# Performance work log

Measured on AMD Instinct MI355X. Metric: run time of the kernel, lower is better.

## Reference

```python
import jax, jax.numpy as jnp
import numpy as np

D_MODEL = 512
N_HEADS = 8
D_K = D_MODEL // N_HEADS
B = 16
S = 1024


def setup_inputs() -> dict:
    key = jax.random.key(0)
    ks = jax.random.split(key, 9)
    xavier = (2.0 / (D_MODEL + D_MODEL)) ** 0.5  # xavier_normal std for square proj
    x = jax.random.normal(ks[0], (B, S, D_MODEL), dtype=jnp.float32)
    Wq = jax.random.normal(ks[1], (D_MODEL, D_MODEL), dtype=jnp.float32) * xavier
    Wk = jax.random.normal(ks[2], (D_MODEL, D_MODEL), dtype=jnp.float32) * xavier
    Wv = jax.random.normal(ks[3], (D_MODEL, D_MODEL), dtype=jnp.float32) * xavier
    Wo = jax.random.normal(ks[4], (D_MODEL, D_MODEL), dtype=jnp.float32) * xavier
    bq = jnp.zeros((D_MODEL,), jnp.float32)
    bk = jnp.zeros((D_MODEL,), jnp.float32)
    bv = jnp.zeros((D_MODEL,), jnp.float32)
    bo = jnp.zeros((D_MODEL,), jnp.float32)
    return {"x": x, "Wq": Wq, "bq": bq, "Wk": Wk, "bk": bk,
            "Wv": Wv, "bv": bv, "Wo": Wo, "bo": bo}


def reference(x, Wq, bq, Wk, bk, Wv, bv, Wo, bo):
    # x: (B, S, D). Projections (nn.Linear applies x @ W.T + b; here W stored as (in,out)).
    b, s, _ = x.shape
    def split_heads(t):  # (B,S,D) -> (B,H,S,dk)
        return t.reshape(b, s, N_HEADS, D_K).transpose(0, 2, 1, 3)
    Q = split_heads(x @ Wq + bq)
    K = split_heads(x @ Wk + bk)
    V = split_heads(x @ Wv + bv)
    scale = 1.0 / jnp.sqrt(jnp.asarray(D_K, x.dtype))
    scores = jnp.einsum('bhqd,bhkd->bhqk', Q, K) * scale
    attn_weights = jax.nn.softmax(scores, axis=-1)
    # dropout is identity in eval mode
    ctx = jnp.einsum('bhqk,bhkd->bhqd', attn_weights, V)
    ctx = ctx.transpose(0, 2, 1, 3).reshape(b, s, D_MODEL)
    out = ctx @ Wo + bo
    return out, attn_weights
```

## Files before the change

kernel.cpp:

```cpp
#include <hip/hip_runtime.h>
#include <stdint.h>

#define D_MODELC 512
#define N_HEADSC 8
#define DKH 64
#define BATCH 16
#define SEQ 1024
#define M_TOT (BATCH*SEQ)
#define NBH (BATCH*N_HEADSC)

typedef __attribute__((ext_vector_type(8))) short short8;
typedef __attribute__((ext_vector_type(4))) float float4v;
typedef __attribute__((ext_vector_type(4))) unsigned short ushort4v;

__device__ inline unsigned short f2bf(float f) {
    unsigned u = __float_as_uint(f);
    u += 0x7FFFu + ((u >> 16) & 1u);
    return (unsigned short)(u >> 16);
}

__device__ inline void gl2lds16(const void* g, void* l) {
    __builtin_amdgcn_global_load_lds(
        (__attribute__((address_space(1))) void*)g,
        (__attribute__((address_space(3))) void*)l, 16, 0, 0);
}

__global__ void k_cvt_x(const float* __restrict__ x, unsigned short* __restrict__ xb) {
    int i = (blockIdx.x * 256 + threadIdx.x) * 4;
    float4v v = *(const float4v*)(x + i);
    ushort4v o;
    o.x = f2bf(v.x); o.y = f2bf(v.y); o.z = f2bf(v.z); o.w = f2bf(v.w);
    *(ushort4v*)(xb + i) = o;
}

__global__ void k_wt(const float* __restrict__ Wq, const float* __restrict__ Wk,
                     const float* __restrict__ Wv, const float* __restrict__ Wo,
                     unsigned short* __restrict__ Wqkvt, unsigned short* __restrict__ Wot) {
    __shared__ float tile[32][33];
    const int blk = blockIdx.x;
    const int mat = blk >> 8;
    const int t2  = blk & 255;
    const int kt = (t2 >> 4) * 32;
    const int nt = (t2 & 15) * 32;
    const float* W = mat == 0 ? Wq : mat == 1 ? Wk : mat == 2 ? Wv : Wo;
    const int tid = threadIdx.x;
    const int cx = tid & 31, ry = tid >> 5;
#pragma unroll
    for (int p = 0; p < 4; ++p) {
        int kr = ry + p * 8;
        tile[kr][cx] = W[(size_t)(kt + kr) * 512 + nt + cx];
    }
    __syncthreads();
    unsigned short* DST = (mat < 3) ? (Wqkvt + (size_t)mat * 512 * 512) : Wot;
#pragma unroll
    for (int p = 0; p < 4; ++p) {
        int nr = ry + p * 8;
        DST[(size_t)(nt + nr) * 512 + kt + cx] = f2bf(tile[cx][nr]);
    }
}

template<int MODE>
__global__ __launch_bounds__(256, 2) void k_gemm(
    const unsigned short* __restrict__ A,
    const unsigned short* __restrict__ Bt,
    const float* __restrict__ bias0,
    const float* __restrict__ bias1,
    const float* __restrict__ bias2,
    unsigned short* __restrict__ Qb,
    unsigned short* __restrict__ Kb,
    unsigned short* __restrict__ Vtb,
    float* __restrict__ Out)
{
    __shared__ __align__(16) unsigned short As[128 * 32];
    __shared__ __align__(16) unsigned short Bs[128 * 32];
    const int m0 = blockIdx.y * 128;
    const int n0 = blockIdx.x * 128;
    const int tid = threadIdx.x;
    const int w = tid >> 6, l = tid & 63;
    const int lm = l & 15, q4 = l >> 4;
    const int wm = (w >> 1) * 64, wn = (w & 1) * 64;

    float4v acc[4][4] = {};

    for (int k0 = 0; k0 < 512; k0 += 32) {
#pragma unroll
        for (int r = 0; r < 2; ++r) {
            int e = tid * 8 + r * 2048;
            int row = e >> 5, col = e & 31;
            gl2lds16(A  + (size_t)(m0 + row) * 512 + k0 + col,
                     (char*)As + w * 1024 + r * 4096);
            gl2lds16(Bt + (size_t)(n0 + row) * 512 + k0 + col,
                     (char*)Bs + w * 1024 + r * 4096);
        }
        __syncthreads();
        short8 af[4], bfr[4];
#pragma unroll
        for (int mi = 0; mi < 4; ++mi)
            af[mi] = *(const short8*)(As + (wm + mi * 16 + lm) * 32 + q4 * 8);
#pragma unroll
        for (int ni = 0; ni < 4; ++ni)
            bfr[ni] = *(const short8*)(Bs + (wn + ni * 16 + lm) * 32 + q4 * 8);
#pragma unroll
        for (int mi = 0; mi < 4; ++mi)
#pragma unroll
            for (int ni = 0; ni < 4; ++ni)
                acc[mi][ni] = __builtin_amdgcn_mfma_f32_16x16x32_bf16(
                    af[mi], bfr[ni], acc[mi][ni], 0, 0, 0);
        __syncthreads();
    }

#pragma unroll
    for (int mi = 0; mi < 4; ++mi)
#pragma unroll
        for (int ni = 0; ni < 4; ++ni)
#pragma unroll
            for (int r = 0; r < 4; ++r) {
                int m = m0 + wm + mi * 16 + q4 * 4 + r;
                int n = n0 + wn + ni * 16 + lm;
                float v = acc[mi][ni][r];
                if (MODE == 0) {
                    int which = n >> 9;
                    int nn = n & 511;
                    int h = nn >> 6, d = nn & 63;
                    int b = m >> 10, s = m & 1023;
                    size_t qkoff = (((size_t)(b * N_HEADSC + h)) * SEQ + s) * DKH + d;
                    if (which == 0) {
                        v = (v + bias0[nn]) * 0.125f;
                        Qb[qkoff] = f2bf(v);
                    } else if (which == 1) {
                        Kb[qkoff] = f2bf(v + bias1[nn]);
                    } else {
                        Vtb[(((size_t)(b * N_HEADSC + h)) * DKH + d) * SEQ + s] =
                            f2bf(v + bias2[nn]);
                    }
                } else {
                    Out[(size_t)m * 512 + n] = v + bias0[n];
                }
            }
}

__global__ __launch_bounds__(256, 2) void k_attn(
    const unsigned short* __restrict__ Qb,
    const unsigned short* __restrict__ Kb,
    float* __restrict__ attn)
{
    __shared__ float wstat[4][32];
    const int blk = blockIdx.x;
    const int bh = blk >> 5;
    const int m0 = (blk & 31) * 32;
    const int tid = threadIdx.x;
    const int w = tid >> 6, l = tid & 63;
    const int lm = l & 15, q4 = l >> 4;
    const unsigned short* Qh = Qb + (size_t)bh * SEQ * DKH;
    const unsigned short* Kh = Kb + (size_t)bh * SEQ * DKH;
    const int nw0 = w * 256;

    short8 a[2][2];
#pragma unroll
    for (int mi = 0; mi < 2; ++mi)
#pragma unroll
        for (int ks = 0; ks < 2; ++ks)
            a[mi][ks] = *(const short8*)(Qh + (size_t)(m0 + mi * 16 + lm) * 64 + ks * 32 + q4 * 8);

    float4v acc[2][16];
#pragma unroll
    for (int cg = 0; cg < 16; ++cg) {
        const unsigned short* kp = Kh + (size_t)(nw0 + cg * 16 + lm) * 64 + q4 * 8;
        short8 b0 = *(const short8*)kp;
        short8 b1 = *(const short8*)(kp + 32);
#pragma unroll
        for (int mi = 0; mi < 2; ++mi) {
            float4v z = {0.f, 0.f, 0.f, 0.f};
            z = __builtin_amdgcn_mfma_f32_16x16x32_bf16(a[mi][0], b0, z, 0, 0, 0);
            acc[mi][cg] = __builtin_amdgcn_mfma_f32_16x16x32_bf16(a[mi][1], b1, z, 0, 0, 0);
        }
    }

    float gM[2][4];
#pragma unroll
    for (int mi = 0; mi < 2; ++mi)
#pragma unroll
        for (int r = 0; r < 4; ++r) {
            float pm = -1e30f;
#pragma unroll
            for (int cg = 0; cg < 16; ++cg) pm = fmaxf(pm, acc[mi][cg][r]);
#pragma unroll
            for (int sh = 1; sh < 16; sh <<= 1) pm = fmaxf(pm, __shfl_xor(pm, sh));
            gM[mi][r] = pm;
        }
    if (lm == 0) {
#pragma unroll
        for (int mi = 0; mi < 2; ++mi)
#pragma unroll
            for (int r = 0; r < 4; ++r)
                wstat[w][mi * 16 + q4 * 4 + r] = gM[mi][r];
    }
    __syncthreads();
#pragma unroll
    for (int mi = 0; mi < 2; ++mi)
#pragma unroll
        for (int r = 0; r < 4; ++r) {
            int row = mi * 16 + q4 * 4 + r;
            gM[mi][r] = fmaxf(fmaxf(wstat[0][row], wstat[1][row]),
                              fmaxf(wstat[2][row], wstat[3][row]));
        }
    __syncthreads();

    float gS[2][4];
#pragma unroll
    for (int mi = 0; mi < 2; ++mi)
#pragma unroll
        for (int r = 0; r < 4; ++r) {
            float ps = 0.f;
#pragma unroll
            for (int cg = 0; cg < 16; ++cg) {
                float e = __expf(acc[mi][cg][r] - gM[mi][r]);
                acc[mi][cg][r] = e;
                ps += e;
            }
#pragma unroll
            for (int sh = 1; sh < 16; sh <<= 1) ps += __shfl_xor(ps, sh);
            gS[mi][r] = ps;
        }
    if (lm == 0) {
#pragma unroll
        for (int mi = 0; mi < 2; ++mi)
#pragma unroll
            for (int r = 0; r < 4; ++r)
                wstat[w][mi * 16 + q4 * 4 + r] = gS[mi][r];
    }
    __syncthreads();
    float inv[2][4];
#pragma unroll
    for (int mi = 0; mi < 2; ++mi)
#pragma unroll
        for (int r = 0; r < 4; ++r) {
            int row = mi * 16 + q4 * 4 + r;
            inv[mi][r] = 1.f / (wstat[0][row] + wstat[1][row] + wstat[2][row] + wstat[3][row]);
        }

    const size_t base = (size_t)bh * SEQ * SEQ;
#pragma unroll
    for (int cg = 0; cg < 16; ++cg)
#pragma unroll
        for (int mi = 0; mi < 2; ++mi)
#pragma unroll
            for (int r = 0; r < 4; ++r)
                attn[base + (size_t)(m0 + mi * 16 + q4 * 4 + r) * SEQ + nw0 + cg * 16 + lm] =
                    acc[mi][cg][r] * inv[mi][r];
}

__global__ __launch_bounds__(256, 2) void k_pv(
    const float* __restrict__ attn,
    const unsigned short* __restrict__ Vtb,
    unsigned short* __restrict__ ctx)
{
    const int blk = blockIdx.x;
    const int bh = blk >> 3;
    const int m0 = (blk & 7) * 128;
    const int tid = threadIdx.x;
    const int w = tid >> 6, l = tid & 63;
    const int lm = l & 15, q4 = l >> 4;
    const float* Ph = attn + (size_t)bh * SEQ * SEQ;
    const unsigned short* Vh = Vtb + (size_t)bh * DKH * SEQ;
    const int wm = w * 32;

    float4v acc[2][4] = {};
    for (int kc = 0; kc < 1024; kc += 32) {
        short8 a[2];
#pragma unroll
        for (int mi = 0; mi < 2; ++mi) {
            const float* p = Ph + (size_t)(m0 + wm + mi * 16 + lm) * SEQ + kc + q4 * 8;
            float4v p0 = *(const float4v*)p;
            float4v p1 = *(const float4v*)(p + 4);
            short8 t;
            t[0] = (short)f2bf(p0.x); t[1] = (short)f2bf(p0.y);
            t[2] = (short)f2bf(p0.z); t[3] = (short)f2bf(p0.w);
            t[4] = (short)f2bf(p1.x); t[5] = (short)f2bf(p1.y);
            t[6] = (short)f2bf(p1.z); t[7] = (short)f2bf(p1.w);
            a[mi] = t;
        }
#pragma unroll
        for (int ni = 0; ni < 4; ++ni) {
            short8 bfr = *(const short8*)(Vh + (size_t)(ni * 16 + lm) * SEQ + kc + q4 * 8);
#pragma unroll
            for (int mi = 0; mi < 2; ++mi)
                acc[mi][ni] = __builtin_amdgcn_mfma_f32_16x16x32_bf16(a[mi], bfr, acc[mi][ni], 0, 0, 0);
        }
    }
    const int bb = bh >> 3, h = bh & 7;
#pragma unroll
    for (int mi = 0; mi < 2; ++mi)
#pragma unroll
        for (int ni = 0; ni < 4; ++ni)
#pragma unroll
            for (int r = 0; r < 4; ++r) {
                int s = m0 + wm + mi * 16 + q4 * 4 + r;
                int d = ni * 16 + lm;
                ctx[((size_t)(bb * SEQ + s)) * 512 + h * 64 + d] = f2bf(acc[mi][ni][r]);
            }
}

extern "C" void kernel_launch(void* const* d_in, const int* in_sizes, int n_in,
                              void* d_out, int out_size, void* d_ws, size_t ws_size,
                              hipStream_t stream) {
    const float* x  = (const float*)d_in[0];
    const float* Wq = (const float*)d_in[1];
    const float* bq = (const float*)d_in[2];
    const float* Wk = (const float*)d_in[3];
    const float* bk = (const float*)d_in[4];
    const float* Wv = (const float*)d_in[5];
    const float* bv = (const float*)d_in[6];
    const float* Wo = (const float*)d_in[7];
    const float* bo = (const float*)d_in[8];

    float* out  = (float*)d_out;
    float* attn = out + (size_t)M_TOT * D_MODELC;

    char* ws = (char*)d_ws;
    unsigned short* xb    = (unsigned short*)(ws);
    unsigned short* Qb    = (unsigned short*)(ws + (size_t)(16u << 20));
    unsigned short* Kb    = (unsigned short*)(ws + (size_t)(32u << 20));
    unsigned short* Vtb   = (unsigned short*)(ws + (size_t)(48u << 20));
    unsigned short* ctxb  = (unsigned short*)(ws + (size_t)(64u << 20));
    unsigned short* Wqkvt = (unsigned short*)(ws + (size_t)(80u << 20));
    unsigned short* Wot   = (unsigned short*)(ws + (size_t)(82u << 20));

    k_cvt_x<<<8192, 256, 0, stream>>>(x, xb);
    k_wt<<<1024, 256, 0, stream>>>(Wq, Wk, Wv, Wo, Wqkvt, Wot);
    k_gemm<0><<<dim3(12, 128), 256, 0, stream>>>(xb, Wqkvt, bq, bk, bv,
                                                 Qb, Kb, Vtb, nullptr);
    k_attn<<<4096, 256, 0, stream>>>(Qb, Kb, attn);
    k_pv<<<1024, 256, 0, stream>>>(attn, Vtb, ctxb);
    k_gemm<1><<<dim3(4, 128), 256, 0, stream>>>(ctxb, Wot, bo, nullptr, nullptr,
                                                nullptr, nullptr, nullptr, out);
}
```

Measured before the change: 951.8 us.

## Fuse PV matmul into attention kernel using LDS-staged bf16 probabilities

Merges the softmax/attention-weights kernel and the P·V kernel into one. Each block writes the normalized probabilities to global memory as before and also stores them as bf16 in a swizzled LDS buffer. It then computes the context for its 32 query rows directly from LDS, so the separate kernel no longer has to re-read the 512MB fp32 attention matrix. The cost is 64KB of LDS per block, which may lower occupancy below the declared two blocks per CU. V is also re-read per 32-row block instead of per 128-row block.

```diff
diff --git a/kernel.cpp b/kernel.cpp
--- a/kernel.cpp
+++ b/kernel.cpp
@@ -139,20 +139,24 @@
             }
 }
 
-__global__ __launch_bounds__(256, 2) void k_attn(
+__global__ __launch_bounds__(256, 2) void k_attn_pv(
     const unsigned short* __restrict__ Qb,
     const unsigned short* __restrict__ Kb,
-    float* __restrict__ attn)
+    const unsigned short* __restrict__ Vtb,
+    float* __restrict__ attn,
+    unsigned short* __restrict__ ctx)
 {
     __shared__ float wstat[4][32];
+    __shared__ __align__(16) unsigned short Pl[4][32 * 256];
     const int blk = blockIdx.x;
     const int bh = blk >> 5;
     const int m0 = (blk & 31) * 32;
     const int tid = threadIdx.x;
     const int w = tid >> 6, l = tid & 63;
     const int lm = l & 15, q4 = l >> 4;
-    const unsigned short* Qh = Qb + (size_t)bh * SEQ * DKH;
-    const unsigned short* Kh = Kb + (size_t)bh * SEQ * DKH;
+    const unsigned short* Qh = Qb  + (size_t)bh * SEQ * DKH;
+    const unsigned short* Kh = Kb  + (size_t)bh * SEQ * DKH;
+    const unsigned short* Vh = Vtb + (size_t)bh * DKH * SEQ;
     const int nw0 = w * 256;
 
     short8 a[2][2];
@@ -240,65 +244,49 @@
         }
 
     const size_t base = (size_t)bh * SEQ * SEQ;
-#pragma unroll
-    for (int cg = 0; cg < 16; ++cg)
-#pragma unroll
-        for (int mi = 0; mi < 2; ++mi)
-#pragma unroll
-            for (int r = 0; r < 4; ++r)
-                attn[base + (size_t)(m0 + mi * 16 + q4 * 4 + r) * SEQ + nw0 + cg * 16 + lm] =
-                    acc[mi][cg][r] * inv[mi][r];
-}
-
-__global__ __launch_bounds__(256, 2) void k_pv(
-    const float* __restrict__ attn,
-    const unsigned short* __restrict__ Vtb,
-    unsigned short* __restrict__ ctx)
-{
-    const int blk = blockIdx.x;
-    const int bh = blk >> 3;
-    const int m0 = (blk & 7) * 128;
-    const int tid = threadIdx.x;
-    const int w = tid >> 6, l = tid & 63;
-    const int lm = l & 15, q4 = l >> 4;
-    const float* Ph = attn + (size_t)bh * SEQ * SEQ;
-    const unsigned short* Vh = Vtb + (size_t)bh * DKH * SEQ;
-    const int wm = w * 32;
-
-    float4v acc[2][4] = {};
-    for (int kc = 0; kc < 1024; kc += 32) {
-        short8 a[2];
-#pragma unroll
-        for (int mi = 0; mi < 2; ++mi) {
-            const float* p = Ph + (size_t)(m0 + wm + mi * 16 + lm) * SEQ + kc + q4 * 8;
-            float4v p0 = *(const float4v*)p;
-            float4v p1 = *(const float4v*)(p + 4);
-            short8 t;
-            t[0] = (short)f2bf(p0.x); t[1] = (short)f2bf(p0.y);
-            t[2] = (short)f2bf(p0.z); t[3] = (short)f2bf(p0.w);
-            t[4] = (short)f2bf(p1.x); t[5] = (short)f2bf(p1.y);
-            t[6] = (short)f2bf(p1.z); t[7] = (short)f2bf(p1.w);
-            a[mi] = t;
-        }
-#pragma unroll
-        for (int ni = 0; ni < 4; ++ni) {
-            short8 bfr = *(const short8*)(Vh + (size_t)(ni * 16 + lm) * SEQ + kc + q4 * 8);
-#pragma unroll
-            for (int mi = 0; mi < 2; ++mi)
-                acc[mi][ni] = __builtin_amdgcn_mfma_f32_16x16x32_bf16(a[mi], bfr, acc[mi][ni], 0, 0, 0);
+    char* Pw = (char*)&Pl[w][0];
+#pragma unroll
+    for (int mi = 0; mi < 2; ++mi)
+#pragma unroll
+        for (int r = 0; r < 4; ++r) {
+            const int row = mi * 16 + q4 * 4 + r;
+            const int rx = (row & 7) << 4;
+            const float iv = inv[mi][r];
+            float* arow = attn + base + (size_t)(m0 + row) * SEQ + nw0;
+#pragma unroll
+            for (int cg = 0; cg < 16; ++cg) {
+                float p = acc[mi][cg][r] * iv;
+                arow[cg * 16 + lm] = p;
+                *(unsigned short*)(Pw + row * 512 + (((cg * 16 + lm) * 2) ^ rx)) = f2bf(p);
+            }
+        }
+    __syncthreads();
+
+    const int rt = w & 1, dt = w >> 1;
+    const int prow = rt * 16 + lm;
+    const int prx  = (prow & 7) << 4;
+    float4v pv[2] = {};
+    for (int kc = 0; kc < 32; ++kc) {
+        const int c    = kc >> 3;
+        const int kloc = (kc & 7) * 32 + q4 * 8;
+        const char* Pc = (const char*)&Pl[c][0];
+        short8 af = *(const short8*)(Pc + prow * 512 + ((kloc * 2) ^ prx));
+        const int kg = kc * 32 + q4 * 8;
+#pragma unroll
+        for (int ni = 0; ni < 2; ++ni) {
+            short8 bfr = *(const short8*)(Vh + (size_t)(dt * 32 + ni * 16 + lm) * SEQ + kg);
+            pv[ni] = __builtin_amdgcn_mfma_f32_16x16x32_bf16(af, bfr, pv[ni], 0, 0, 0);
         }
     }
     const int bb = bh >> 3, h = bh & 7;
 #pragma unroll
-    for (int mi = 0; mi < 2; ++mi)
-#pragma unroll
-        for (int ni = 0; ni < 4; ++ni)
-#pragma unroll
-            for (int r = 0; r < 4; ++r) {
-                int s = m0 + wm + mi * 16 + q4 * 4 + r;
-                int d = ni * 16 + lm;
-                ctx[((size_t)(bb * SEQ + s)) * 512 + h * 64 + d] = f2bf(acc[mi][ni][r]);
-            }
+    for (int ni = 0; ni < 2; ++ni)
+#pragma unroll
+        for (int r = 0; r < 4; ++r) {
+            int s = m0 + rt * 16 + q4 * 4 + r;
+            int d = dt * 32 + ni * 16 + lm;
+            ctx[((size_t)(bb * SEQ + s)) * 512 + h * 64 + d] = f2bf(pv[ni][r]);
+        }
 }
 
 extern "C" void kernel_launch(void* const* d_in, const int* in_sizes, int n_in,
@@ -330,8 +318,7 @@
     k_wt<<<1024, 256, 0, stream>>>(Wq, Wk, Wv, Wo, Wqkvt, Wot);
     k_gemm<0><<<dim3(12, 128), 256, 0, stream>>>(xb, Wqkvt, bq, bk, bv,
                                                  Qb, Kb, Vtb, nullptr);
-    k_attn<<<4096, 256, 0, stream>>>(Qb, Kb, attn);
-    k_pv<<<1024, 256, 0, stream>>>(attn, Vtb, ctxb);
+    k_attn_pv<<<4096, 256, 0, stream>>>(Qb, Kb, Vtb, attn, ctxb);
     k_gemm<1><<<dim3(4, 128), 256, 0, stream>>>(ctxb, Wot, bo, nullptr, nullptr,
                                                 nullptr, nullptr, nullptr, out);
 }
```

Result: faster. 858.7 us (-9.8%).
